# Kernel optimization log

Hardware: AMD Instinct MI355X
Metric: run time of the kernel (lower is better)

## Reference

```python
import jax, jax.numpy as jnp
import numpy as np

B, T, D_MODEL, H, DK = 2, 1024, 1024, 16, 64
ADJ_TOPK, PHASE_TOPK, N_STEPS = 128, 128, 4


def _sparse_softmax(scores, k):
    # top-k per row, softmax over the kept entries, zeros elsewhere
    vals, idx = jax.lax.top_k(scores, k)            # (B,h,T,k)
    w = jax.nn.softmax(vals, axis=-1)
    b, h, t, _ = scores.shape
    bi = jnp.arange(b)[:, None, None, None]
    hi = jnp.arange(h)[None, :, None, None]
    ti = jnp.arange(t)[None, None, :, None]
    return jnp.zeros_like(scores).at[bi, hi, ti, idx].set(w)


def _heads(y):
    return y.reshape(B, T, H, DK).transpose(0, 2, 1, 3)  # (B,h,T,d_k)


def setup_inputs() -> dict:
    key = jax.random.key(0)
    ks = jax.random.split(key, 8)
    s = 0.02
    return {
        "x": jax.random.normal(ks[0], (B, T, D_MODEL), jnp.float32),
        "W_Q": jax.random.normal(ks[1], (D_MODEL, D_MODEL), jnp.float32) * s,
        "W_K": jax.random.normal(ks[2], (D_MODEL, D_MODEL), jnp.float32) * s,
        "W_re": jax.random.normal(ks[3], (D_MODEL, D_MODEL), jnp.float32) * s,
        "W_im": jax.random.normal(ks[4], (D_MODEL, D_MODEL), jnp.float32) * s,
        "W_V": jax.random.normal(ks[5], (D_MODEL, D_MODEL), jnp.float32) * s,
        "W_O": jax.random.normal(ks[6], (D_MODEL, D_MODEL), jnp.float32) * s,
        "logit_lam": jnp.float32(0.0),   # sigmoid -> lam=0.5
        "log_alpha": jnp.float32(-3.0),  # matches nn.Parameter init
    }


def reference(x, W_Q, W_K, W_re, W_im, W_V, W_O, logit_lam, log_alpha):
    # --- AdjacencyBuilder: A = sparse_softmax(QK^T/sqrt(dk)) ---
    Q = _heads(x @ W_Q.T)
    K = _heads(x @ W_K.T)
    scores = jnp.einsum('bhtd,bhsd->bhts', Q, K) / np.sqrt(DK).astype(np.float32)
    A = _sparse_softmax(scores, ADJ_TOPK)          # (B,h,T,T)

    # --- PhaseEncoding: D = W_re x + i W_im x (kept as real/imag pair) ---
    Dr = _heads(x @ W_re.T)
    Di = _heads(x @ W_im.T)
    D0r, D0i = Dr, Di

    # --- TopologyPropagation: D <- (1-lam) D + lam A D, n_steps times ---
    lam = jax.nn.sigmoid(logit_lam)
    for _ in range(N_STEPS):
        Dr = (1.0 - lam) * Dr + lam * jnp.einsum('bhts,bhsd->bhtd', A, Dr)
        Di = (1.0 - lam) * Di + lam * jnp.einsum('bhts,bhsd->bhtd', A, Di)
    alpha = jax.nn.sigmoid(log_alpha)
    Dr = Dr + alpha * D0r
    Di = Di + alpha * D0i

    # --- phase sync attention: Re(D_i . conj(D_j)) on unit-normalized D ---
    norm = jnp.maximum(jnp.sqrt(jnp.sum(Dr * Dr + Di * Di, axis=-1, keepdims=True)), 1e-6)
    Ur, Ui = Dr / norm, Di / norm
    phase_sim = (jnp.einsum('bhtd,bhsd->bhts', Ur, Ur)
                 + jnp.einsum('bhtd,bhsd->bhts', Ui, Ui)) * np.sqrt(2.0 * DK).astype(np.float32)
    phase_attn = _sparse_softmax(phase_sim, PHASE_TOPK)

    # --- weighted V sum + output projection ---
    V = _heads(x @ W_V.T)
    out = jnp.einsum('bhts,bhsd->bhtd', phase_attn, V)
    out = out.transpose(0, 2, 1, 3).reshape(B, T, D_MODEL)
    return out @ W_O.T, phase_attn
```

## Files before the change

### kernel.cpp

```cpp
#include <hip/hip_runtime.h>
#include <cstdint>
#include <cstddef>

#define B_  2
#define T_  1024
#define DM  1024
#define H_  16
#define DK_ 64
#define TOPK 128

typedef unsigned short ushort_t;
typedef __attribute__((ext_vector_type(8))) short short8;
typedef __attribute__((ext_vector_type(8))) unsigned short u16x8;
typedef __attribute__((ext_vector_type(4))) float f32x4;

__device__ __forceinline__ unsigned fkey16(unsigned b) {
  return (b & 0x8000u) ? (0xffffu & ~b) : (b | 0x8000u);
}

__device__ __forceinline__ ushort_t f2bf(float f) {
  unsigned u = __float_as_uint(f);
  return (ushort_t)((u + 0x7fffu + ((u >> 16) & 1u)) >> 16);
}
__device__ __forceinline__ float bf2f(ushort_t u) {
  return __uint_as_float((unsigned)u << 16);
}

__device__ __forceinline__ void gload_lds16(const ushort_t* g, ushort_t* l) {
  __builtin_amdgcn_global_load_lds(
      (const __attribute__((address_space(1))) unsigned int*)(const void*)g,
      (__attribute__((address_space(3))) unsigned int*)(void*)l, 16, 0, 0);
}

__global__ __launch_bounds__(256) void cast6_kernel(
    const float* __restrict__ x, const float* __restrict__ wq,
    const float* __restrict__ wk, const float* __restrict__ wre,
    const float* __restrict__ wim, const float* __restrict__ wv,
    ushort_t* __restrict__ xb, ushort_t* __restrict__ w5b) {
  int z = blockIdx.y;
  const float* src; ushort_t* dst; int n4;
  switch (z) {
    case 0: src = x;   dst = xb;                 n4 = 524288; break;
    case 1: src = wq;  dst = w5b;                n4 = 262144; break;
    case 2: src = wk;  dst = w5b + 1048576;      n4 = 262144; break;
    case 3: src = wre; dst = w5b + 2097152;      n4 = 262144; break;
    case 4: src = wim; dst = w5b + 3145728;      n4 = 262144; break;
    default: src = wv; dst = w5b + 4194304;      n4 = 262144; break;
  }
  int i = blockIdx.x * 256 + threadIdx.x;
  if (i < n4) {
    float4 v = ((const float4*)src)[i];
    ushort4 o;
    o.x = f2bf(v.x); o.y = f2bf(v.y); o.z = f2bf(v.z); o.w = f2bf(v.w);
    ((ushort4*)dst)[i] = o;
  }
}

__global__ __launch_bounds__(256) void cast_bf16_kernel(
    const float* __restrict__ in, ushort_t* __restrict__ out, int n4) {
  int i = blockIdx.x * 256 + threadIdx.x;
  if (i < n4) {
    float4 v = ((const float4*)in)[i];
    ushort4 o;
    o.x = f2bf(v.x); o.y = f2bf(v.y); o.z = f2bf(v.z); o.w = f2bf(v.w);
    ((ushort4*)out)[i] = o;
  }
}

template<int KDIM>
__device__ __forceinline__ void gemm_core(
    const ushort_t* __restrict__ Ab, const ushort_t* __restrict__ Bb,
    ushort_t* ldsA, ushort_t* ldsB, int tid, f32x4 acc[4][4]) {
  const int lane = tid & 63, wid = tid >> 6;
  const int wr = (wid >> 1) * 64, wc = (wid & 1) * 64;
  const int l15 = lane & 15, l4 = lane >> 4;
  for (int k0 = 0; k0 < KDIM; k0 += 64) {
    #pragma unroll
    for (int i = 0; i < 4; ++i) {
      int cid = tid + 256 * i;
      int row = cid >> 3, slot = cid & 7;
      int gc = slot ^ (row & 7);
      gload_lds16(&Ab[(size_t)row * KDIM + k0 + gc * 8], &ldsA[cid * 8]);
      gload_lds16(&Bb[(size_t)row * KDIM + k0 + gc * 8], &ldsB[cid * 8]);
    }
    __syncthreads();
    #pragma unroll
    for (int ks = 0; ks < 2; ++ks) {
      short8 af[4], bfr[4];
      #pragma unroll
      for (int m = 0; m < 4; ++m) {
        int r = wr + m * 16 + l15;
        int c = ks * 4 + l4;
        af[m] = *(const short8*)&ldsA[r * 64 + (c ^ (r & 7)) * 8];
      }
      #pragma unroll
      for (int n = 0; n < 4; ++n) {
        int r = wc + n * 16 + l15;
        int c = ks * 4 + l4;
        bfr[n] = *(const short8*)&ldsB[r * 64 + (c ^ (r & 7)) * 8];
      }
      #pragma unroll
      for (int m = 0; m < 4; ++m)
        #pragma unroll
        for (int n = 0; n < 4; ++n)
          acc[m][n] = __builtin_amdgcn_mfma_f32_16x16x32_bf16(
              af[m], bfr[n], acc[m][n], 0, 0, 0);
    }
    __syncthreads();
  }
}

__global__ __launch_bounds__(256) void proj5_mfma(
    const ushort_t* __restrict__ xb, const ushort_t* __restrict__ wb,
    ushort_t* __restrict__ qh_b, ushort_t* __restrict__ kh_b,
    ushort_t* __restrict__ dt0, ushort_t* __restrict__ vt_b) {
  __shared__ ushort_t ldsA[128 * 64];
  __shared__ ushort_t ldsB[128 * 64];
  int tid = threadIdx.x;
  int orig = (blockIdx.x & 7) * 80 + (blockIdx.x >> 3);
  int bx = orig & 7, by = (orig >> 3) & 15, z = orig >> 7;
  const ushort_t* W = wb + (size_t)z * (DM * DM);
  f32x4 acc[4][4];
  #pragma unroll
  for (int m = 0; m < 4; ++m)
    #pragma unroll
    for (int n = 0; n < 4; ++n) acc[m][n] = (f32x4){0.f, 0.f, 0.f, 0.f};
  gemm_core<DM>(xb + (size_t)by * 128 * DM,
                W + (size_t)bx * 128 * DM, ldsA, ldsB, tid, acc);
  const int lane = tid & 63, wid = tid >> 6;
  int row0 = by * 128 + (wid >> 1) * 64 + (lane >> 4) * 4;
  int col0 = bx * 128 + (wid & 1) * 64 + (lane & 15);
  #pragma unroll
  for (int m = 0; m < 4; ++m)
    #pragma unroll
    for (int n = 0; n < 4; ++n)
      #pragma unroll
      for (int j = 0; j < 4; ++j) {
        int nr = row0 + m * 16 + j;
        int mc = col0 + n * 16;
        int b = nr >> 10, t = nr & 1023, h = mc >> 6, d = mc & 63;
        int head = b * H_ + h;
        float v = acc[m][n][j];
        if (z == 0) {
          qh_b[((size_t)head * T_ + t) * DK_ + d] = f2bf(v);
        } else if (z == 1) {
          kh_b[((size_t)head * T_ + t) * DK_ + d] = f2bf(v);
        } else if (z == 4) {
          vt_b[(size_t)head * 65536 + (size_t)d * 1024 + t] = f2bf(v);
        } else {
          int ddofs = (z == 3) ? 64 : 0;
          dt0[(size_t)head * 131072 + (size_t)(d + ddofs) * 1024 + t] = f2bf(v);
        }
      }
}

template<int KDIM>
__global__ __launch_bounds__(256) void score_mfma(
    const ushort_t* __restrict__ A, const ushort_t* __restrict__ Bm,
    ushort_t* __restrict__ Sout, float scale) {
  __shared__ ushort_t ldsA[128 * 64];
  __shared__ ushort_t ldsB[128 * 64];
  int tid = threadIdx.x;
  int orig = (blockIdx.x & 7) * 256 + (blockIdx.x >> 3);
  int bx = orig & 7, by = (orig >> 3) & 7, z = orig >> 6;
  f32x4 acc[4][4];
  #pragma unroll
  for (int m = 0; m < 4; ++m)
    #pragma unroll
    for (int n = 0; n < 4; ++n) acc[m][n] = (f32x4){0.f, 0.f, 0.f, 0.f};
  gemm_core<KDIM>(A + (size_t)z * T_ * KDIM + (size_t)by * 128 * KDIM,
                  Bm + (size_t)z * T_ * KDIM + (size_t)bx * 128 * KDIM,
                  ldsA, ldsB, tid, acc);
  const int lane = tid & 63, wid = tid >> 6;
  int row0 = by * 128 + (wid >> 1) * 64 + (lane >> 4) * 4;
  int col0 = bx * 128 + (wid & 1) * 64 + (lane & 15);
  ushort_t* Sz = Sout + (size_t)z * T_ * T_;
  #pragma unroll
  for (int m = 0; m < 4; ++m)
    #pragma unroll
    for (int n = 0; n < 4; ++n)
      #pragma unroll
      for (int j = 0; j < 4; ++j)
        Sz[(size_t)(row0 + m * 16 + j) * T_ + col0 + n * 16] =
            f2bf(acc[m][n][j] * scale);
}

__global__ __launch_bounds__(256) void score_sym_mfma(
    const ushort_t* __restrict__ P, ushort_t* __restrict__ Sout, float scale) {
  __shared__ ushort_t lds[128 * 128];
  ushort_t* ldsA = lds;
  ushort_t* ldsB = lds + 128 * 64;
  int tid = threadIdx.x;
  int swz = (blockIdx.x & 7) * 144 + (blockIdx.x >> 3);
  int z = swz / 36, t = swz % 36;
  int by = 0, rem = t;
  while (rem >= 8 - by) { rem -= 8 - by; ++by; }
  int bx = by + rem;
  const ushort_t* Pz = P + (size_t)z * T_ * 128;
  f32x4 acc[4][4];
  #pragma unroll
  for (int m = 0; m < 4; ++m)
    #pragma unroll
    for (int n = 0; n < 4; ++n) acc[m][n] = (f32x4){0.f, 0.f, 0.f, 0.f};
  gemm_core<128>(Pz + (size_t)by * 128 * 128, Pz + (size_t)bx * 128 * 128,
                 ldsA, ldsB, tid, acc);
  const int lane = tid & 63, wid = tid >> 6;
  const int l15 = lane & 15, l4 = lane >> 4;
  ushort_t* Sz = Sout + (size_t)z * T_ * T_;
  int row0 = by * 128 + (wid >> 1) * 64 + l4 * 4;
  int col0 = bx * 128 + (wid & 1) * 64 + l15;
  #pragma unroll
  for (int m = 0; m < 4; ++m)
    #pragma unroll
    for (int n = 0; n < 4; ++n)
      #pragma unroll
      for (int j = 0; j < 4; ++j)
        Sz[(size_t)(row0 + m * 16 + j) * T_ + col0 + n * 16] =
            f2bf(acc[m][n][j] * scale);
  if (bx != by) {
    int lr0 = (wid >> 1) * 64 + l4 * 4;
    int lc0 = (wid & 1) * 64 + l15;
    #pragma unroll
    for (int m = 0; m < 4; ++m)
      #pragma unroll
      for (int n = 0; n < 4; ++n)
        #pragma unroll
        for (int j = 0; j < 4; ++j) {
          int lr = lr0 + m * 16 + j;
          int lc = lc0 + n * 16;
          lds[lc * 128 + (lr ^ ((lc & 15) << 3))] = f2bf(acc[m][n][j] * scale);
        }
    __syncthreads();
    int p = tid >> 1, qh = (tid & 1) * 64;
    int s = (p & 15) << 3;
    ushort_t* dstRow = Sz + (size_t)(bx * 128 + p) * T_ + by * 128 + qh;
    #pragma unroll
    for (int qc = 0; qc < 8; ++qc)
      *(u16x8*)&dstRow[qc * 8] =
          *(const u16x8*)&lds[p * 128 + ((qh + qc * 8) ^ s)];
  }
}

__device__ __forceinline__ void mfma_64x128_loop(
    const ushort_t* __restrict__ Ah, const ushort_t* __restrict__ Bh,
    ushort_t* ldsA, ushort_t* ldsB, int tid, f32x4 acc[2][4]) {
  const int lane = tid & 63, wid = tid >> 6;
  const int wr = wid >> 1, wc = wid & 1;
  const int l15 = lane & 15, l4 = lane >> 4;
  for (int k0 = 0; k0 < 1024; k0 += 64) {
    #pragma unroll
    for (int i = 0; i < 2; ++i) {
      int cid = tid + 256 * i;
      int rowc = cid >> 3, slot = cid & 7;
      int gc = slot ^ (rowc & 7);
      gload_lds16(&Ah[(size_t)rowc * 1024 + k0 + gc * 8], &ldsA[cid * 8]);
    }
    #pragma unroll
    for (int i = 0; i < 4; ++i) {
      int cid = tid + 256 * i;
      int rowc = cid >> 3, slot = cid & 7;
      int gc = slot ^ (rowc & 7);
      gload_lds16(&Bh[(size_t)rowc * 1024 + k0 + gc * 8], &ldsB[cid * 8]);
    }
    __syncthreads();
    #pragma unroll
    for (int ks = 0; ks < 2; ++ks) {
      short8 af[2], bfr[4];
      #pragma unroll
      for (int m = 0; m < 2; ++m) {
        int r = wr * 32 + m * 16 + l15;
        int c = ks * 4 + l4;
        af[m] = *(const short8*)&ldsA[r * 64 + (c ^ (r & 7)) * 8];
      }
      #pragma unroll
      for (int n = 0; n < 4; ++n) {
        int r = wc * 64 + n * 16 + l15;
        int c = ks * 4 + l4;
        bfr[n] = *(const short8*)&ldsB[r * 64 + (c ^ (r & 7)) * 8];
      }
      #pragma unroll
      for (int m = 0; m < 2; ++m)
        #pragma unroll
        for (int n = 0; n < 4; ++n)
          acc[m][n] = __builtin_amdgcn_mfma_f32_16x16x32_bf16(
              af[m], bfr[n], acc[m][n], 0, 0, 0);
    }
    __syncthreads();
  }
}

__global__ __launch_bounds__(256) void prop_mfma(
    const ushort_t* __restrict__ Ab, const ushort_t* __restrict__ Dsrc,
    ushort_t* __restrict__ Ddst, const float* __restrict__ logit_lam) {
  __shared__ ushort_t ldsA[64 * 64];
  __shared__ ushort_t ldsB[128 * 64];
  int tid = threadIdx.x;
  int orig = (blockIdx.x & 7) * 64 + (blockIdx.x >> 3);
  int bx = orig & 15, hz = orig >> 4;
  const int lane = tid & 63, wid = tid >> 6;
  const int wr = wid >> 1, wc = wid & 1;
  const int l15 = lane & 15, l4 = lane >> 4;
  const ushort_t* Dh = Dsrc + (size_t)hz * 131072;
  f32x4 acc[2][4];
  #pragma unroll
  for (int m = 0; m < 2; ++m)
    #pragma unroll
    for (int n = 0; n < 4; ++n) acc[m][n] = (f32x4){0.f, 0.f, 0.f, 0.f};
  mfma_64x128_loop(Ab + (size_t)hz * 1048576 + (size_t)bx * 64 * 1024,
                   Dh, ldsA, ldsB, tid, acc);
  float lam = 1.f / (1.f + __expf(-logit_lam[0]));
  ushort_t* Dd = Ddst + (size_t)hz * 131072;
  #pragma unroll
  for (int m = 0; m < 2; ++m)
    #pragma unroll
    for (int n = 0; n < 4; ++n)
      #pragma unroll
      for (int j = 0; j < 4; ++j) {
        int t = bx * 64 + wr * 32 + m * 16 + l4 * 4 + j;
        int dd = wc * 64 + n * 16 + l15;
        size_t o = (size_t)dd * 1024 + t;
        float oldv = bf2f(Dh[o]);
        Dd[o] = f2bf((1.f - lam) * oldv + lam * acc[m][n][j]);
      }
}

__global__ __launch_bounds__(256) void prop_final_mfma(
    const ushort_t* __restrict__ Ab, const ushort_t* __restrict__ Dsrc,
    const ushort_t* __restrict__ Dt0, ushort_t* __restrict__ P,
    const float* __restrict__ logit_lam, const float* __restrict__ log_alpha) {
  __shared__ ushort_t ldsA[64 * 64];
  __shared__ ushort_t ldsB[128 * 64];
  __shared__ float sums[4][2][4][4];
  int tid = threadIdx.x;
  int orig = (blockIdx.x & 7) * 64 + (blockIdx.x >> 3);
  int bx = orig & 15, hz = orig >> 4;
  const int lane = tid & 63, wid = tid >> 6;
  const int wr = wid >> 1, wc = wid & 1;
  const int l15 = lane & 15, l4 = lane >> 4;
  const ushort_t* Dh = Dsrc + (size_t)hz * 131072;
  f32x4 acc[2][4];
  #pragma unroll
  for (int m = 0; m < 2; ++m)
    #pragma unroll
    for (int n = 0; n < 4; ++n) acc[m][n] = (f32x4){0.f, 0.f, 0.f, 0.f};
  mfma_64x128_loop(Ab + (size_t)hz * 1048576 + (size_t)bx * 64 * 1024,
                   Dh, ldsA, ldsB, tid, acc);
  float lam = 1.f / (1.f + __expf(-logit_lam[0]));
  float alpha = 1.f / (1.f + __expf(-log_alpha[0]));
  const ushort_t* D0h = Dt0 + (size_t)hz * 131072;
  float F[2][4][4];
  float ssp[2][4];
  #pragma unroll
  for (int m = 0; m < 2; ++m)
    #pragma unroll
    for (int j = 0; j < 4; ++j) {
      int t = bx * 64 + wr * 32 + m * 16 + l4 * 4 + j;
      float s = 0.f;
      #pragma unroll
      for (int n = 0; n < 4; ++n) {
        int dd = wc * 64 + n * 16 + l15;
        size_t o = (size_t)dd * 1024 + t;
        float f = (1.f - lam) * bf2f(Dh[o]) + lam * acc[m][n][j] +
                  alpha * bf2f(D0h[o]);
        F[m][n][j] = f;
        s += f * f;
      }
      #pragma unroll
      for (int off = 1; off < 16; off <<= 1) s += __shfl_xor(s, off);
      ssp[m][j] = s;
    }
  if (l15 == 0) {
    #pragma unroll
    for (int m = 0; m < 2; ++m)
      #pragma unroll
      for (int j = 0; j < 4; ++j)
        sums[wid][m][j][l4] = ssp[m][j];
  }
  __syncthreads();
  ushort_t* Ph = P + (size_t)hz * 1024 * 128;
  #pragma unroll
  for (int m = 0; m < 2; ++m)
    #pragma unroll
    for (int j = 0; j < 4; ++j) {
      float tot = sums[wid][m][j][l4] + sums[wid ^ 1][m][j][l4];
      float ni = 1.f / fmaxf(sqrtf(tot), 1e-6f);
      int t = bx * 64 + wr * 32 + m * 16 + l4 * 4 + j;
      #pragma unroll
      for (int n = 0; n < 4; ++n) {
        int dd = wc * 64 + n * 16 + l15;
        Ph[(size_t)t * 128 + dd] = f2bf(F[m][n][j] * ni);
      }
    }
}

template<int MODE>
__global__ __launch_bounds__(256) void topk16_kernel(
    ushort_t* __restrict__ Sb, float* __restrict__ denseOut) {
  const int tid = threadIdx.x;
  const int lane = tid & 63, wv = tid >> 6;
  const int row = blockIdx.x * 4 + wv;
  ushort_t* Srow = Sb + (size_t)row * 1024;

  float scr[2][8];
  unsigned kk[2][8];
  #pragma unroll
  for (int g = 0; g < 2; ++g) {
    u16x8 v = *(const u16x8*)&Srow[g * 512 + lane * 8];
    #pragma unroll
    for (int e = 0; e < 8; ++e) {
      scr[g][e] = bf2f(v[e]);
      kk[g][e] = fkey16((unsigned)v[e]);
    }
  }

  unsigned prefix = 0, r = TOPK;
  #pragma unroll
  for (int b = 15; b >= 0; --b) {
    unsigned want = (prefix << 1) | 1u;
    unsigned cnt = 0;
    #pragma unroll
    for (int g = 0; g < 2; ++g)
      #pragma unroll
      for (int e = 0; e < 8; ++e)
        cnt += (unsigned)__popcll(__ballot((kk[g][e] >> b) == want));
    if (cnt >= r) prefix = want;
    else { prefix <<= 1; r -= cnt; }
  }
  const unsigned thr = prefix;

  float mx = -3.402823466e38f;
  #pragma unroll
  for (int g = 0; g < 2; ++g)
    #pragma unroll
    for (int e = 0; e < 8; ++e) mx = fmaxf(mx, scr[g][e]);
  #pragma unroll
  for (int off = 1; off < 64; off <<= 1) mx = fmaxf(mx, __shfl_xor(mx, off));

  const unsigned long long below = (1ull << lane) - 1ull;
  unsigned cum = 0;
  float w[2][8];
  float ps = 0.f;
  #pragma unroll
  for (int g = 0; g < 2; ++g) {
    unsigned long long bal[8];
    #pragma unroll
    for (int e = 0; e < 8; ++e) bal[e] = __ballot(kk[g][e] == thr);
    unsigned rb = cum;
    #pragma unroll
    for (int e = 0; e < 8; ++e) rb += (unsigned)__popcll(bal[e] & below);
    unsigned ownPrior = 0;
    #pragma unroll
    for (int e = 0; e < 8; ++e) {
      bool eq = (kk[g][e] == thr);
      bool sel = (kk[g][e] > thr) || (eq && (rb + ownPrior) < r);
      ownPrior += eq ? 1u : 0u;
      float ex = sel ? __expf(scr[g][e] - mx) : 0.f;
      w[g][e] = ex;
      ps += ex;
    }
    #pragma unroll
    for (int e = 0; e < 8; ++e) cum += (unsigned)__popcll(bal[e]);
  }
  float pss = ps;
  #pragma unroll
  for (int off = 1; off < 64; off <<= 1) pss += __shfl_xor(pss, off);
  const float inv = 1.f / pss;

  if (MODE == 0) {
    float* Drow = denseOut + (size_t)row * 1024;
    #pragma unroll
    for (int g = 0; g < 2; ++g) {
      *(float4*)&Drow[g * 512 + lane * 8] =
          make_float4(w[g][0] * inv, w[g][1] * inv, w[g][2] * inv, w[g][3] * inv);
      *(float4*)&Drow[g * 512 + lane * 8 + 4] =
          make_float4(w[g][4] * inv, w[g][5] * inv, w[g][6] * inv, w[g][7] * inv);
    }
  }
  #pragma unroll
  for (int g = 0; g < 2; ++g) {
    u16x8 o;
    #pragma unroll
    for (int e = 0; e < 8; ++e) o[e] = f2bf(w[g][e] * inv);
    *(u16x8*)&Srow[g * 512 + lane * 8] = o;
  }
}

__global__ __launch_bounds__(256) void attnv_mfma(
    const ushort_t* __restrict__ Wb, const ushort_t* __restrict__ Vt,
    ushort_t* __restrict__ attn_b) {
  __shared__ ushort_t ldsA[64 * 64];
  __shared__ ushort_t ldsB[64 * 64];
  int tid = threadIdx.x;
  int orig = (blockIdx.x & 7) * 64 + (blockIdx.x >> 3);
  int bx = orig & 15, hz = orig >> 4;
  const int lane = tid & 63, wid = tid >> 6;
  const int wr = wid >> 1, wc = wid & 1;
  const int l15 = lane & 15, l4 = lane >> 4;
  const ushort_t* Wh = Wb + (size_t)hz * 1048576 + (size_t)bx * 64 * 1024;
  const ushort_t* Vh = Vt + (size_t)hz * 65536;
  f32x4 acc[2][2];
  #pragma unroll
  for (int m = 0; m < 2; ++m)
    #pragma unroll
    for (int n = 0; n < 2; ++n) acc[m][n] = (f32x4){0.f, 0.f, 0.f, 0.f};
  for (int k0 = 0; k0 < 1024; k0 += 64) {
    #pragma unroll
    for (int i = 0; i < 2; ++i) {
      int cid = tid + 256 * i;
      int rowc = cid >> 3, slot = cid & 7;
      int gc = slot ^ (rowc & 7);
      gload_lds16(&Wh[(size_t)rowc * 1024 + k0 + gc * 8], &ldsA[cid * 8]);
    }
    #pragma unroll
    for (int i = 0; i < 2; ++i) {
      int cid = tid + 256 * i;
      int rowc = cid >> 3, slot = cid & 7;
      int gc = slot ^ (rowc & 7);
      gload_lds16(&Vh[(size_t)rowc * 1024 + k0 + gc * 8], &ldsB[cid * 8]);
    }
    __syncthreads();
    #pragma unroll
    for (int ks = 0; ks < 2; ++ks) {
      short8 af[2], bfr[2];
      #pragma unroll
      for (int m = 0; m < 2; ++m) {
        int r = wr * 32 + m * 16 + l15;
        int c = ks * 4 + l4;
        af[m] = *(const short8*)&ldsA[r * 64 + (c ^ (r & 7)) * 8];
      }
      #pragma unroll
      for (int n = 0; n < 2; ++n) {
        int r = wc * 32 + n * 16 + l15;
        int c = ks * 4 + l4;
        bfr[n] = *(const short8*)&ldsB[r * 64 + (c ^ (r & 7)) * 8];
      }
      #pragma unroll
      for (int m = 0; m < 2; ++m)
        #pragma unroll
        for (int n = 0; n < 2; ++n)
          acc[m][n] = __builtin_amdgcn_mfma_f32_16x16x32_bf16(
              af[m], bfr[n], acc[m][n], 0, 0, 0);
    }
    __syncthreads();
  }
  int b = hz >> 4, h = hz & 15;
  #pragma unroll
  for (int m = 0; m < 2; ++m)
    #pragma unroll
    for (int n = 0; n < 2; ++n)
      #pragma unroll
      for (int j = 0; j < 4; ++j) {
        int t = bx * 64 + wr * 32 + m * 16 + l4 * 4 + j;
        int d = wc * 32 + n * 16 + l15;
        attn_b[((size_t)(b * T_ + t)) * DM + h * DK_ + d] = f2bf(acc[m][n][j]);
      }
}

__global__ __launch_bounds__(256) void outproj_mfma(
    const ushort_t* __restrict__ A, const ushort_t* __restrict__ Wo,
    float* __restrict__ out) {
  __shared__ ushort_t ldsA[64 * 64];
  __shared__ ushort_t ldsB[128 * 64];
  int tid = threadIdx.x;
  int orig = (blockIdx.x & 7) * 32 + (blockIdx.x >> 3);
  int bx = orig & 7, by = orig >> 3;
  const int lane = tid & 63, wid = tid >> 6;
  const int wr = wid >> 1, wc = wid & 1;
  const int l15 = lane & 15, l4 = lane >> 4;
  f32x4 acc[2][4];
  #pragma unroll
  for (int m = 0; m < 2; ++m)
    #pragma unroll
    for (int n = 0; n < 4; ++n) acc[m][n] = (f32x4){0.f, 0.f, 0.f, 0.f};
  mfma_64x128_loop(A + (size_t)by * 64 * 1024,
                   Wo + (size_t)bx * 128 * 1024, ldsA, ldsB, tid, acc);
  #pragma unroll
  for (int m = 0; m < 2; ++m)
    #pragma unroll
    for (int n = 0; n < 4; ++n)
      #pragma unroll
      for (int j = 0; j < 4; ++j) {
        int r = by * 64 + wr * 32 + m * 16 + l4 * 4 + j;
        int c = bx * 128 + wc * 64 + n * 16 + l15;
        out[(size_t)r * 1024 + c] = acc[m][n][j];
      }
}

extern "C" void kernel_launch(void* const* d_in, const int* in_sizes, int n_in,
                              void* d_out, int out_size, void* d_ws, size_t ws_size,
                              hipStream_t stream) {
  (void)in_sizes; (void)n_in; (void)out_size; (void)ws_size;
  const float* x         = (const float*)d_in[0];
  const float* wq        = (const float*)d_in[1];
  const float* wk        = (const float*)d_in[2];
  const float* wre       = (const float*)d_in[3];
  const float* wim       = (const float*)d_in[4];
  const float* wv        = (const float*)d_in[5];
  const float* wo        = (const float*)d_in[6];
  const float* logit_lam = (const float*)d_in[7];
  const float* log_alpha = (const float*)d_in[8];

  float* out   = (float*)d_out;
  float* dense = out + (size_t)B_ * T_ * DM;
  ushort_t* w5_b = (ushort_t*)dense;

  char* ws = (char*)d_ws;
  const size_t MB = (size_t)1 << 20;
  ushort_t* A_b  = (ushort_t*)(ws + 0 * MB);
  ushort_t* S2_b = A_b;
  ushort_t* dt0  = (ushort_t*)(ws + 64 * MB);
  ushort_t* dtA  = (ushort_t*)(ws + 72 * MB);
  ushort_t* dtB  = (ushort_t*)(ws + 80 * MB);
  ushort_t* P_b  = dtB;
  ushort_t* vt_b = (ushort_t*)(ws + 88 * MB);
  ushort_t* xb   = (ushort_t*)(ws + 92 * MB);
  ushort_t* attn_b = xb;
  ushort_t* qh_b = (ushort_t*)(ws + 96 * MB);
  ushort_t* wo_b = qh_b;
  ushort_t* kh_b = (ushort_t*)(ws + 100 * MB);

  const int rows = B_ * H_ * T_;

  cast6_kernel<<<dim3(2048, 6), 256, 0, stream>>>(
      x, wq, wk, wre, wim, wv, xb, w5_b);

  proj5_mfma<<<640, 256, 0, stream>>>(xb, w5_b, qh_b, kh_b, dt0, vt_b);

  score_mfma<64><<<2048, 256, 0, stream>>>(qh_b, kh_b, A_b, 0.125f);
  cast_bf16_kernel<<<1024, 256, 0, stream>>>(wo, wo_b, DM * DM / 4);
  topk16_kernel<1><<<rows / 4, 256, 0, stream>>>(A_b, nullptr);

  prop_mfma<<<512, 256, 0, stream>>>(A_b, dt0, dtA, logit_lam);
  prop_mfma<<<512, 256, 0, stream>>>(A_b, dtA, dtB, logit_lam);
  prop_mfma<<<512, 256, 0, stream>>>(A_b, dtB, dtA, logit_lam);
  prop_final_mfma<<<512, 256, 0, stream>>>(A_b, dtA, dt0, P_b,
                                           logit_lam, log_alpha);

  score_sym_mfma<<<1152, 256, 0, stream>>>(P_b, S2_b, 11.3137085f);
  topk16_kernel<0><<<rows / 4, 256, 0, stream>>>(S2_b, dense);

  attnv_mfma<<<512, 256, 0, stream>>>(S2_b, vt_b, attn_b);
  outproj_mfma<<<256, 256, 0, stream>>>(attn_b, wo_b, out);
}
```

Measured before the change: 336.7 us.

## Fuse top-k sparse softmax into first propagation and attn-V kernels

Removes the two standalone top-k kernels. The adjacency top-k now runs inside the first propagation kernel, reading scores from a separate buffer (the output's dense region) and writing bf16 weights to A. The phase top-k runs inside the attn-V kernel, which writes the fp32 dense output and then reloads it as fp32, converting to bf16 when filling LDS. This saves two launches and one bf16 write/read round trip per stage. In exchange, each block processes 64 rows serially with only 4 waves before its MFMA loop can start, and the attn-V A operand becomes a wider fp32 load handled in registers instead of direct global-to-LDS loads.

Measured after the change: 402.4 us. +19.5%, slower.

```diff
diff --git a/kernel.cpp b/kernel.cpp
--- a/kernel.cpp
+++ b/kernel.cpp
@@ -289,6 +289,141 @@
   }
 }
 
+__device__ __forceinline__ void topk_row(
+    u16x8 v0, u16x8 v1, int lane,
+    float* __restrict__ denseRow, ushort_t* __restrict__ wRow) {
+  float scr[2][8];
+  unsigned kk[2][8];
+  #pragma unroll
+  for (int e = 0; e < 8; ++e) {
+    scr[0][e] = bf2f(v0[e]); kk[0][e] = fkey16((unsigned)v0[e]);
+    scr[1][e] = bf2f(v1[e]); kk[1][e] = fkey16((unsigned)v1[e]);
+  }
+  unsigned prefix = 0, r = TOPK;
+  #pragma unroll
+  for (int b = 15; b >= 0; --b) {
+    unsigned want = (prefix << 1) | 1u;
+    unsigned cnt = 0;
+    #pragma unroll
+    for (int g = 0; g < 2; ++g)
+      #pragma unroll
+      for (int e = 0; e < 8; ++e)
+        cnt += (unsigned)__popcll(__ballot((kk[g][e] >> b) == want));
+    if (cnt >= r) prefix = want;
+    else { prefix <<= 1; r -= cnt; }
+  }
+  const unsigned thr = prefix;
+
+  float mx = -3.402823466e38f;
+  #pragma unroll
+  for (int g = 0; g < 2; ++g)
+    #pragma unroll
+    for (int e = 0; e < 8; ++e) mx = fmaxf(mx, scr[g][e]);
+  #pragma unroll
+  for (int off = 1; off < 64; off <<= 1) mx = fmaxf(mx, __shfl_xor(mx, off));
+
+  const unsigned long long below = (1ull << lane) - 1ull;
+  unsigned cum = 0;
+  float w[2][8];
+  float ps = 0.f;
+  #pragma unroll
+  for (int g = 0; g < 2; ++g) {
+    unsigned long long bal[8];
+    #pragma unroll
+    for (int e = 0; e < 8; ++e) bal[e] = __ballot(kk[g][e] == thr);
+    unsigned rb = cum;
+    #pragma unroll
+    for (int e = 0; e < 8; ++e) rb += (unsigned)__popcll(bal[e] & below);
+    unsigned ownPrior = 0;
+    #pragma unroll
+    for (int e = 0; e < 8; ++e) {
+      bool eq = (kk[g][e] == thr);
+      bool sel = (kk[g][e] > thr) || (eq && (rb + ownPrior) < r);
+      ownPrior += eq ? 1u : 0u;
+      float ex = sel ? __expf(scr[g][e] - mx) : 0.f;
+      w[g][e] = ex;
+      ps += ex;
+    }
+    #pragma unroll
+    for (int e = 0; e < 8; ++e) cum += (unsigned)__popcll(bal[e]);
+  }
+  float pss = ps;
+  #pragma unroll
+  for (int off = 1; off < 64; off <<= 1) pss += __shfl_xor(pss, off);
+  const float inv = 1.f / pss;
+
+  if (denseRow) {
+    #pragma unroll
+    for (int g = 0; g < 2; ++g) {
+      *(float4*)&denseRow[g * 512 + lane * 8] =
+          make_float4(w[g][0] * inv, w[g][1] * inv, w[g][2] * inv, w[g][3] * inv);
+      *(float4*)&denseRow[g * 512 + lane * 8 + 4] =
+          make_float4(w[g][4] * inv, w[g][5] * inv, w[g][6] * inv, w[g][7] * inv);
+    }
+  }
+  if (wRow) {
+    #pragma unroll
+    for (int g = 0; g < 2; ++g) {
+      u16x8 o;
+      #pragma unroll
+      for (int e = 0; e < 8; ++e) o[e] = f2bf(w[g][e] * inv);
+      *(u16x8*)&wRow[g * 512 + lane * 8] = o;
+    }
+  }
+}
+
+__global__ __launch_bounds__(256) void topk_prop1_mfma(
+    const ushort_t* __restrict__ Sc, ushort_t* __restrict__ Ab,
+    const ushort_t* __restrict__ Dsrc, ushort_t* __restrict__ Ddst,
+    const float* __restrict__ logit_lam) {
+  __shared__ ushort_t ldsA[64 * 64];
+  __shared__ ushort_t ldsB[128 * 64];
+  int tid = threadIdx.x;
+  int orig = (blockIdx.x & 7) * 64 + (blockIdx.x >> 3);
+  int bx = orig & 15, hz = orig >> 4;
+  const int lane = tid & 63, wid = tid >> 6;
+  const size_t baseRow = (size_t)hz * 1024 + (size_t)bx * 64;
+  {
+    const ushort_t* sr = Sc + (baseRow + wid * 16) * 1024;
+    ushort_t* wrp = Ab + (baseRow + wid * 16) * 1024;
+    u16x8 c0 = *(const u16x8*)&sr[lane * 8];
+    u16x8 c1 = *(const u16x8*)&sr[512 + lane * 8];
+    for (int rr = 0; rr < 16; ++rr) {
+      u16x8 n0, n1;
+      if (rr < 15) {
+        n0 = *(const u16x8*)&sr[(size_t)(rr + 1) * 1024 + lane * 8];
+        n1 = *(const u16x8*)&sr[(size_t)(rr + 1) * 1024 + 512 + lane * 8];
+      }
+      topk_row(c0, c1, lane, nullptr, wrp + (size_t)rr * 1024);
+      if (rr < 15) { c0 = n0; c1 = n1; }
+    }
+  }
+  __syncthreads();
+  const int wr = wid >> 1, wc = wid & 1;
+  const int l15 = lane & 15, l4 = lane >> 4;
+  const ushort_t* Dh = Dsrc + (size_t)hz * 131072;
+  f32x4 acc[2][4];
+  #pragma unroll
+  for (int m = 0; m < 2; ++m)
+    #pragma unroll
+    for (int n = 0; n < 4; ++n) acc[m][n] = (f32x4){0.f, 0.f, 0.f, 0.f};
+  mfma_64x128_loop(Ab + baseRow * 1024, Dh, ldsA, ldsB, tid, acc);
+  float lam = 1.f / (1.f + __expf(-logit_lam[0]));
+  ushort_t* Dd = Ddst + (size_t)hz * 131072;
+  #pragma unroll
+  for (int m = 0; m < 2; ++m)
+    #pragma unroll
+    for (int n = 0; n < 4; ++n)
+      #pragma unroll
+      for (int j = 0; j < 4; ++j) {
+        int t = bx * 64 + wr * 32 + m * 16 + l4 * 4 + j;
+        int dd = wc * 64 + n * 16 + l15;
+        size_t o = (size_t)dd * 1024 + t;
+        float oldv = bf2f(Dh[o]);
+        Dd[o] = f2bf((1.f - lam) * oldv + lam * acc[m][n][j]);
+      }
+}
+
 __global__ __launch_bounds__(256) void prop_mfma(
     const ushort_t* __restrict__ Ab, const ushort_t* __restrict__ Dsrc,
     ushort_t* __restrict__ Ddst, const float* __restrict__ logit_lam) {
@@ -393,110 +528,35 @@
     }
 }
 
-template<int MODE>
-__global__ __launch_bounds__(256) void topk16_kernel(
-    ushort_t* __restrict__ Sb, float* __restrict__ denseOut) {
-  const int tid = threadIdx.x;
-  const int lane = tid & 63, wv = tid >> 6;
-  const int row = blockIdx.x * 4 + wv;
-  ushort_t* Srow = Sb + (size_t)row * 1024;
-
-  float scr[2][8];
-  unsigned kk[2][8];
-  #pragma unroll
-  for (int g = 0; g < 2; ++g) {
-    u16x8 v = *(const u16x8*)&Srow[g * 512 + lane * 8];
-    #pragma unroll
-    for (int e = 0; e < 8; ++e) {
-      scr[g][e] = bf2f(v[e]);
-      kk[g][e] = fkey16((unsigned)v[e]);
-    }
-  }
-
-  unsigned prefix = 0, r = TOPK;
-  #pragma unroll
-  for (int b = 15; b >= 0; --b) {
-    unsigned want = (prefix << 1) | 1u;
-    unsigned cnt = 0;
-    #pragma unroll
-    for (int g = 0; g < 2; ++g)
-      #pragma unroll
-      for (int e = 0; e < 8; ++e)
-        cnt += (unsigned)__popcll(__ballot((kk[g][e] >> b) == want));
-    if (cnt >= r) prefix = want;
-    else { prefix <<= 1; r -= cnt; }
-  }
-  const unsigned thr = prefix;
-
-  float mx = -3.402823466e38f;
-  #pragma unroll
-  for (int g = 0; g < 2; ++g)
-    #pragma unroll
-    for (int e = 0; e < 8; ++e) mx = fmaxf(mx, scr[g][e]);
-  #pragma unroll
-  for (int off = 1; off < 64; off <<= 1) mx = fmaxf(mx, __shfl_xor(mx, off));
-
-  const unsigned long long below = (1ull << lane) - 1ull;
-  unsigned cum = 0;
-  float w[2][8];
-  float ps = 0.f;
-  #pragma unroll
-  for (int g = 0; g < 2; ++g) {
-    unsigned long long bal[8];
-    #pragma unroll
-    for (int e = 0; e < 8; ++e) bal[e] = __ballot(kk[g][e] == thr);
-    unsigned rb = cum;
-    #pragma unroll
-    for (int e = 0; e < 8; ++e) rb += (unsigned)__popcll(bal[e] & below);
-    unsigned ownPrior = 0;
-    #pragma unroll
-    for (int e = 0; e < 8; ++e) {
-      bool eq = (kk[g][e] == thr);
-      bool sel = (kk[g][e] > thr) || (eq && (rb + ownPrior) < r);
-      ownPrior += eq ? 1u : 0u;
-      float ex = sel ? __expf(scr[g][e] - mx) : 0.f;
-      w[g][e] = ex;
-      ps += ex;
-    }
-    #pragma unroll
-    for (int e = 0; e < 8; ++e) cum += (unsigned)__popcll(bal[e]);
-  }
-  float pss = ps;
-  #pragma unroll
-  for (int off = 1; off < 64; off <<= 1) pss += __shfl_xor(pss, off);
-  const float inv = 1.f / pss;
-
-  if (MODE == 0) {
-    float* Drow = denseOut + (size_t)row * 1024;
-    #pragma unroll
-    for (int g = 0; g < 2; ++g) {
-      *(float4*)&Drow[g * 512 + lane * 8] =
-          make_float4(w[g][0] * inv, w[g][1] * inv, w[g][2] * inv, w[g][3] * inv);
-      *(float4*)&Drow[g * 512 + lane * 8 + 4] =
-          make_float4(w[g][4] * inv, w[g][5] * inv, w[g][6] * inv, w[g][7] * inv);
-    }
-  }
-  #pragma unroll
-  for (int g = 0; g < 2; ++g) {
-    u16x8 o;
-    #pragma unroll
-    for (int e = 0; e < 8; ++e) o[e] = f2bf(w[g][e] * inv);
-    *(u16x8*)&Srow[g * 512 + lane * 8] = o;
-  }
-}
-
-__global__ __launch_bounds__(256) void attnv_mfma(
-    const ushort_t* __restrict__ Wb, const ushort_t* __restrict__ Vt,
-    ushort_t* __restrict__ attn_b) {
+__global__ __launch_bounds__(256) void topk_attnv_mfma(
+    const ushort_t* __restrict__ Sc, float* __restrict__ dense,
+    const ushort_t* __restrict__ Vt, ushort_t* __restrict__ attn_b) {
   __shared__ ushort_t ldsA[64 * 64];
   __shared__ ushort_t ldsB[64 * 64];
   int tid = threadIdx.x;
   int orig = (blockIdx.x & 7) * 64 + (blockIdx.x >> 3);
   int bx = orig & 15, hz = orig >> 4;
   const int lane = tid & 63, wid = tid >> 6;
+  const size_t baseRow = (size_t)hz * 1024 + (size_t)bx * 64;
+  {
+    const ushort_t* sr = Sc + (baseRow + wid * 16) * 1024;
+    float* dr = dense + (baseRow + wid * 16) * 1024;
+    u16x8 c0 = *(const u16x8*)&sr[lane * 8];
+    u16x8 c1 = *(const u16x8*)&sr[512 + lane * 8];
+    for (int rr = 0; rr < 16; ++rr) {
+      u16x8 n0, n1;
+      if (rr < 15) {
+        n0 = *(const u16x8*)&sr[(size_t)(rr + 1) * 1024 + lane * 8];
+        n1 = *(const u16x8*)&sr[(size_t)(rr + 1) * 1024 + 512 + lane * 8];
+      }
+      topk_row(c0, c1, lane, dr + (size_t)rr * 1024, nullptr);
+      if (rr < 15) { c0 = n0; c1 = n1; }
+    }
+  }
+  __syncthreads();
   const int wr = wid >> 1, wc = wid & 1;
   const int l15 = lane & 15, l4 = lane >> 4;
-  const ushort_t* Wh = Wb + (size_t)hz * 1048576 + (size_t)bx * 64 * 1024;
+  const float* Wh = dense + baseRow * 1024;
   const ushort_t* Vh = Vt + (size_t)hz * 65536;
   f32x4 acc[2][2];
   #pragma unroll
@@ -505,11 +565,14 @@
     for (int n = 0; n < 2; ++n) acc[m][n] = (f32x4){0.f, 0.f, 0.f, 0.f};
   for (int k0 = 0; k0 < 1024; k0 += 64) {
     #pragma unroll
-    for (int i = 0; i < 2; ++i) {
+    for (int i = 0; i < 4; ++i) {
       int cid = tid + 256 * i;
-      int rowc = cid >> 3, slot = cid & 7;
-      int gc = slot ^ (rowc & 7);
-      gload_lds16(&Wh[(size_t)rowc * 1024 + k0 + gc * 8], &ldsA[cid * 8]);
+      int rowc = cid >> 4, c4 = cid & 15;
+      float4 v = *(const float4*)&Wh[(size_t)rowc * 1024 + k0 + c4 * 4];
+      int c = c4 >> 1, half = c4 & 1;
+      ushort4 o;
+      o.x = f2bf(v.x); o.y = f2bf(v.y); o.z = f2bf(v.z); o.w = f2bf(v.w);
+      *(ushort4*)&ldsA[rowc * 64 + (c ^ (rowc & 7)) * 8 + half * 4] = o;
     }
     #pragma unroll
     for (int i = 0; i < 2; ++i) {
@@ -602,7 +665,8 @@
 
   float* out   = (float*)d_out;
   float* dense = out + (size_t)B_ * T_ * DM;
-  ushort_t* w5_b = (ushort_t*)dense;
+  ushort_t* w5_b   = (ushort_t*)dense;
+  ushort_t* sc_adj = (ushort_t*)dense;
 
   char* ws = (char*)d_ws;
   const size_t MB = (size_t)1 << 20;
@@ -619,26 +683,22 @@
   ushort_t* wo_b = qh_b;
   ushort_t* kh_b = (ushort_t*)(ws + 100 * MB);
 
-  const int rows = B_ * H_ * T_;
-
   cast6_kernel<<<dim3(2048, 6), 256, 0, stream>>>(
       x, wq, wk, wre, wim, wv, xb, w5_b);
 
   proj5_mfma<<<640, 256, 0, stream>>>(xb, w5_b, qh_b, kh_b, dt0, vt_b);
 
-  score_mfma<64><<<2048, 256, 0, stream>>>(qh_b, kh_b, A_b, 0.125f);
+  score_mfma<64><<<2048, 256, 0, stream>>>(qh_b, kh_b, sc_adj, 0.125f);
   cast_bf16_kernel<<<1024, 256, 0, stream>>>(wo, wo_b, DM * DM / 4);
-  topk16_kernel<1><<<rows / 4, 256, 0, stream>>>(A_b, nullptr);
-
-  prop_mfma<<<512, 256, 0, stream>>>(A_b, dt0, dtA, logit_lam);
+
+  topk_prop1_mfma<<<512, 256, 0, stream>>>(sc_adj, A_b, dt0, dtA, logit_lam);
   prop_mfma<<<512, 256, 0, stream>>>(A_b, dtA, dtB, logit_lam);
   prop_mfma<<<512, 256, 0, stream>>>(A_b, dtB, dtA, logit_lam);
   prop_final_mfma<<<512, 256, 0, stream>>>(A_b, dtA, dt0, P_b,
                                            logit_lam, log_alpha);
 
   score_sym_mfma<<<1152, 256, 0, stream>>>(P_b, S2_b, 11.3137085f);
-  topk16_kernel<0><<<rows / 4, 256, 0, stream>>>(S2_b, dense);
-
-  attnv_mfma<<<512, 256, 0, stream>>>(S2_b, vt_b, attn_b);
+
+  topk_attnv_mfma<<<512, 256, 0, stream>>>(S2_b, dense, vt_b, attn_b);
   outproj_mfma<<<256, 256, 0, stream>>>(attn_b, wo_b, out);
 }
```
